# Performance work log

Measured on AMD Instinct MI355X. Metric: run time of the kernel, lower is better.

## Reference

```python
import jax, jax.numpy as jnp
import numpy as np

B, C, F = 16384, 1000, 256
ALPHA = 10


def setup_inputs() -> dict:
    key = jax.random.key(0)
    k1, k2, k3, k4, k5 = jax.random.split(key, 5)
    logits = jax.random.normal(k1, (B, C), dtype=jnp.float32)
    features = jax.random.normal(k2, (B, F), dtype=jnp.float32)
    mean_vecs = jax.random.normal(k3, (C, F), dtype=jnp.float32)
    # Per-class Weibull (shape, loc, scale) as fit by scipy.weibull_min.fit.
    wb_shape = jax.random.uniform(k4, (C,), dtype=jnp.float32, minval=1.0, maxval=4.0)
    wb_loc = jnp.zeros((C,), dtype=jnp.float32)
    # typical tail distance for randn features/means is ~sqrt(2F) ~ 22.6
    wb_scale = jax.random.uniform(k5, (C,), dtype=jnp.float32, minval=10.0, maxval=25.0)
    return {"logits": logits, "features": features, "mean_vecs": mean_vecs,
            "wb_shape": wb_shape, "wb_loc": wb_loc, "wb_scale": wb_scale}


def reference(logits, features, mean_vecs, wb_shape, wb_loc, wb_scale):
    # Batched per-class Euclidean distances via the GEMM identity
    # ||f - m||^2 = ||f||^2 + ||m||^2 - 2 f.m  (avoids [B,C,F] intermediate).
    f2 = jnp.sum(features * features, axis=1, keepdims=True)        # [B,1]
    m2 = jnp.sum(mean_vecs * mean_vecs, axis=1)                     # [C]
    d2 = f2 + m2[None, :] - 2.0 * (features @ mean_vecs.T)          # [B,C]
    dist = jnp.sqrt(jnp.maximum(d2, 1e-12))                         # [B,C]
    # Analytic weibull_min CDF: 1 - exp(-((x - loc)/scale)^c), 0 for x <= loc.
    xp = (dist - wb_loc[None, :]) / wb_scale[None, :]
    pos = xp > 0
    xp_safe = jnp.where(pos, xp, 1.0)
    w = jnp.where(pos, 1.0 - jnp.exp(-(xp_safe ** wb_shape[None, :])), 0.0)
    # OpenMax reweighting + softmax (exp/sum-normalize as in the original).
    scores = logits * (1.0 - w ** ALPHA)                            # [B,C]
    return jax.nn.softmax(scores, axis=-1)
```

## Files before the change

kernel.cpp:

```cpp
#include <hip/hip_runtime.h>

#define NB 16384
#define NC 1000
#define NF 256
#define SE_STRIDE 1004

typedef _Float16 half8 __attribute__((ext_vector_type(8)));
typedef _Float16 half4v __attribute__((ext_vector_type(4)));
typedef float f32x4 __attribute__((ext_vector_type(4)));

__global__ __launch_bounds__(256) void prep_kernel(
    const float* __restrict__ mean_vecs,
    const float* __restrict__ wb_shape,
    const float* __restrict__ wb_loc,
    const float* __restrict__ wb_scale,
    _Float16* __restrict__ m16f,
    float* __restrict__ pm2,
    float* __restrict__ psh,
    float* __restrict__ pli,
    float* __restrict__ pis)
{
    const int lane = threadIdx.x & 63;
    const int W = blockIdx.x * 4 + (threadIdx.x >> 6);

    if (W < 512) {
        const int gt = W >> 3, kk = W & 7;
        int cls = gt * 16 + (lane & 15);
        if (cls > NC - 1) cls = NC - 1;
        const float* src = mean_vecs + (size_t)cls * NF + kk * 32 + (lane >> 4) * 8;
        const float4 lo = *(const float4*)src;
        const float4 hi = *(const float4*)(src + 4);
        half8 h;
        h[0]=(_Float16)lo.x; h[1]=(_Float16)lo.y; h[2]=(_Float16)lo.z; h[3]=(_Float16)lo.w;
        h[4]=(_Float16)hi.x; h[5]=(_Float16)hi.y; h[6]=(_Float16)hi.z; h[7]=(_Float16)hi.w;
        *((half8*)m16f + (size_t)W * 64 + lane) = h;
    }
    if (W < NC) {
        const float4 v = *((const float4*)(mean_vecs + (size_t)W * NF) + lane);
        float s = v.x*v.x + v.y*v.y + v.z*v.z + v.w*v.w;
        #pragma unroll
        for (int off = 1; off < 64; off <<= 1) s += __shfl_xor(s, off, 64);
        if (lane == 0) {
            const float isc = 1.0f / wb_scale[W];
            pm2[W] = s;
            psh[W] = wb_shape[W];
            pli[W] = wb_loc[W] * isc;
            pis[W] = isc;
        }
    }
}

__global__ __launch_bounds__(512, 4) void score_kernel(
    const float* __restrict__ logits,
    const float* __restrict__ features,
    const _Float16* __restrict__ m16f,
    const float* __restrict__ pm2,
    const float* __restrict__ psh,
    const float* __restrict__ pli,
    const float* __restrict__ pis,
    float* __restrict__ out)
{
    __shared__ _Float16 sfeat[8][512];
    __shared__ _Float16 se[16][SE_STRIDE];
    __shared__ float sp[4][1024];
    __shared__ float sf2[16];

    const int lane = threadIdx.x & 63;
    const int wave = threadIdx.x >> 6;
    const int q    = lane >> 4;
    const int mr   = lane & 15;
    const int row  = blockIdx.x * 16 + mr;

    const half8* mbase = (const half8*)m16f + (size_t)(wave * 8) * 8 * 64 + lane;

    half8 aA[8], aB[8];
    #pragma unroll
    for (int kk = 0; kk < 8; ++kk) aA[kk] = mbase[kk * 64];
    #pragma unroll
    for (int kk = 0; kk < 8; ++kk) aB[kk] = mbase[(8 + kk) * 64];

    {
        const int t = threadIdx.x;
        if (t < 256) {
            ((float4*)&sp[0][0])[t] = ((const float4*)pm2)[t];
            ((float4*)&sp[2][0])[t] = ((const float4*)pli)[t];
        } else {
            const int u = t - 256;
            ((float4*)&sp[1][0])[u] = ((const float4*)psh)[u];
            ((float4*)&sp[3][0])[u] = ((const float4*)pis)[u];
        }
    }

    {
        const float* src = features + (size_t)(blockIdx.x * 16 + mr) * NF
                         + wave * 32 + q * 8;
        const float4 lo = *(const float4*)src;
        const float4 hi = *(const float4*)(src + 4);
        half8 h;
        h[0]=(_Float16)lo.x; h[1]=(_Float16)lo.y; h[2]=(_Float16)lo.z; h[3]=(_Float16)lo.w;
        h[4]=(_Float16)hi.x; h[5]=(_Float16)hi.y; h[6]=(_Float16)hi.z; h[7]=(_Float16)hi.w;
        *(half8*)&sfeat[wave][lane * 8] = h;
    }

    if (wave == 0) {
        float f2l = 0.f;
        const float* fb = features + (size_t)row * NF;
        #pragma unroll
        for (int kk = 0; kk < 8; ++kk) {
            const float4* p = (const float4*)(fb + kk * 32 + q * 8);
            const float4 lo = p[0], hi = p[1];
            f2l += lo.x*lo.x + lo.y*lo.y + lo.z*lo.z + lo.w*lo.w
                 + hi.x*hi.x + hi.y*hi.y + hi.z*hi.z + hi.w*hi.w;
        }
        f2l += __shfl_xor(f2l, 16, 64);
        f2l += __shfl_xor(f2l, 32, 64);
        if (lane < 16) sf2[lane] = f2l;
    }

    __syncthreads();

    const float f2 = sf2[mr];
    const float NL2E = -1.44269504088896340736f;
    const float LOG2E = 1.44269504088896340736f;

#define TILE_BODY(T, BUF)                                                     \
    do {                                                                      \
        const int cb   = (wave * 8 + (T)) * 16 + q * 4;                       \
        const bool cvg = (cb <= NC - 4);                                      \
        const int cbc  = cvg ? cb : (NC - 4);                                 \
        f32x4 acc0 = {0.f, 0.f, 0.f, 0.f};                                    \
        f32x4 acc1 = {0.f, 0.f, 0.f, 0.f};                                    \
        _Pragma("unroll")                                                     \
        for (int kk = 0; kk < 4; ++kk) {                                      \
            const half8 b0 = *(const half8*)&sfeat[kk][lane * 8];             \
            const half8 b1 = *(const half8*)&sfeat[kk + 4][lane * 8];         \
            acc0 = __builtin_amdgcn_mfma_f32_16x16x32_f16(BUF[kk],     b0, acc0, 0, 0, 0); \
            acc1 = __builtin_amdgcn_mfma_f32_16x16x32_f16(BUF[kk + 4], b1, acc1, 0, 0, 0); \
        }                                                                     \
        if ((T) + 2 < 8) {                                                    \
            _Pragma("unroll")                                                 \
            for (int kk = 0; kk < 8; ++kk)                                    \
                BUF[kk] = mbase[(size_t)(((T) + 2) * 8 + kk) * 64];           \
        }                                                                     \
        const f32x4 m2v = *(const f32x4*)&sp[0][cbc];                         \
        const f32x4 shv = *(const f32x4*)&sp[1][cbc];                         \
        const f32x4 liv = *(const f32x4*)&sp[2][cbc];                         \
        const f32x4 iv  = *(const f32x4*)&sp[3][cbc];                         \
        half4v oh;                                                            \
        _Pragma("unroll")                                                     \
        for (int j = 0; j < 4; ++j) {                                         \
            float av   = acc0[j] + acc1[j];                                   \
            float d2   = fmaxf(f2 + m2v[j] - 2.0f * av, 1e-12f);              \
            float dist = __builtin_amdgcn_sqrtf(d2);                          \
            float xp   = dist * iv[j] - liv[j];                               \
            float xs   = fmaxf(xp, 1e-30f);                                   \
            float tt   = __builtin_amdgcn_exp2f(                              \
                             shv[j] * __builtin_amdgcn_logf(xs));             \
            float w    = 1.0f - __builtin_amdgcn_exp2f(NL2E * tt);            \
            w = (xp > 0.f) ? w : 0.f;                                         \
            float w2 = w * w, w4 = w2 * w2, w8 = w4 * w4;                     \
            oh[j] = (_Float16)(1.0f - w8 * w2);                               \
        }                                                                     \
        if (cvg)                                                              \
            *(half4v*)&se[mr][cb] = oh;                                       \
    } while (0)

    TILE_BODY(0, aA);
    TILE_BODY(1, aB);
    TILE_BODY(2, aA);
    TILE_BODY(3, aB);
    TILE_BODY(4, aA);
    TILE_BODY(5, aB);
    TILE_BODY(6, aA);
    TILE_BODY(7, aB);
#undef TILE_BODY

    float4 lgp[2][4];
    #pragma unroll
    for (int rr = 0; rr < 2; ++rr) {
        const size_t grow = (size_t)(blockIdx.x * 16 + wave * 2 + rr);
        const float* lrow = logits + grow * NC;
        #pragma unroll
        for (int i = 0; i < 4; ++i) {
            const int idx = i * 64 + lane;
            if (idx < 250) {
                float4 l4 = *(const float4*)(lrow + idx * 4);
                l4.x *= LOG2E; l4.y *= LOG2E; l4.z *= LOG2E; l4.w *= LOG2E;
                lgp[rr][i] = l4;
            }
        }
    }

    __syncthreads();

    #pragma unroll
    for (int rr = 0; rr < 2; ++rr) {
        const int r = wave * 2 + rr;
        const size_t grow = (size_t)(blockIdx.x * 16 + r);

        float4 ev[4];
        float psum = 0.f;
        #pragma unroll
        for (int i = 0; i < 4; ++i) {
            const int idx = i * 64 + lane;
            if (idx < 250) {
                const half4v g4 = *(const half4v*)&se[r][idx * 4];
                const float4 l4 = lgp[rr][i];
                float4 e4;
                e4.x = __builtin_amdgcn_exp2f(l4.x * (float)g4[0]);
                e4.y = __builtin_amdgcn_exp2f(l4.y * (float)g4[1]);
                e4.z = __builtin_amdgcn_exp2f(l4.z * (float)g4[2]);
                e4.w = __builtin_amdgcn_exp2f(l4.w * (float)g4[3]);
                ev[i] = e4;
                psum += (e4.x + e4.y) + (e4.z + e4.w);
            }
        }
        #pragma unroll
        for (int off = 1; off < 64; off <<= 1)
            psum += __shfl_xor(psum, off, 64);
        const float inv = 1.0f / psum;

        float* orow = out + grow * NC;
        #pragma unroll
        for (int i = 0; i < 4; ++i) {
            const int idx = i * 64 + lane;
            if (idx < 250) {
                float4 v = ev[i];
                v.x *= inv; v.y *= inv; v.z *= inv; v.w *= inv;
                *(float4*)(orow + idx * 4) = v;
            }
        }
    }
}

extern "C" void kernel_launch(void* const* d_in, const int* in_sizes, int n_in,
                              void* d_out, int out_size, void* d_ws, size_t ws_size,
                              hipStream_t stream) {
    const float* logits    = (const float*)d_in[0];
    const float* features  = (const float*)d_in[1];
    const float* mean_vecs = (const float*)d_in[2];
    const float* wb_shape  = (const float*)d_in[3];
    const float* wb_loc    = (const float*)d_in[4];
    const float* wb_scale  = (const float*)d_in[5];
    float* out = (float*)d_out;

    _Float16* m16f = (_Float16*)d_ws;
    float* pm2 = (float*)((char*)d_ws + 524288);
    float* psh = (float*)((char*)d_ws + 524288 + 4096);
    float* pli = (float*)((char*)d_ws + 524288 + 8192);
    float* pis = (float*)((char*)d_ws + 524288 + 12288);

    prep_kernel<<<252, 256, 0, stream>>>(mean_vecs, wb_shape, wb_loc, wb_scale,
                                         m16f, pm2, psh, pli, pis);
    score_kernel<<<NB / 16, 512, 0, stream>>>(logits, features, m16f,
                                              pm2, psh, pli, pis, out);
}
```

Before: 156.3 us.

## Parallelize feature norm over four waves, raise MFMA priority, use nontemporal output stores

The per-row squared-norm computation moves from a single wave to four waves, each reducing four rows with coalesced float4 loads and xor shuffles. This shortens the serial prologue before the barrier. The MFMA section is wrapped in s_setprio raise and lower calls so matrix work gets issue priority over other waves. The output softmax rows are written with nontemporal stores to avoid polluting cache with write-once data. These are three independent micro-optimizations, and each has a small, uncertain effect.

```diff
diff --git a/kernel.cpp b/kernel.cpp
--- a/kernel.cpp
+++ b/kernel.cpp
@@ -69,7 +69,6 @@
     const int wave = threadIdx.x >> 6;
     const int q    = lane >> 4;
     const int mr   = lane & 15;
-    const int row  = blockIdx.x * 16 + mr;
 
     const half8* mbase = (const half8*)m16f + (size_t)(wave * 8) * 8 * 64 + lane;
 
@@ -102,19 +101,22 @@
         *(half8*)&sfeat[wave][lane * 8] = h;
     }
 
-    if (wave == 0) {
-        float f2l = 0.f;
-        const float* fb = features + (size_t)row * NF;
-        #pragma unroll
-        for (int kk = 0; kk < 8; ++kk) {
-            const float4* p = (const float4*)(fb + kk * 32 + q * 8);
-            const float4 lo = p[0], hi = p[1];
-            f2l += lo.x*lo.x + lo.y*lo.y + lo.z*lo.z + lo.w*lo.w
-                 + hi.x*hi.x + hi.y*hi.y + hi.z*hi.z + hi.w*hi.w;
-        }
-        f2l += __shfl_xor(f2l, 16, 64);
-        f2l += __shfl_xor(f2l, 32, 64);
-        if (lane < 16) sf2[lane] = f2l;
+    if (wave < 4) {
+        const int r   = wave * 4 + (lane >> 4);
+        const int c16 = lane & 15;
+        const float4* fb = (const float4*)(features
+                          + (size_t)(blockIdx.x * 16 + r) * NF) + c16 * 4;
+        float s = 0.f;
+        #pragma unroll
+        for (int i = 0; i < 4; ++i) {
+            const float4 v = fb[i];
+            s += v.x*v.x + v.y*v.y + v.z*v.z + v.w*v.w;
+        }
+        s += __shfl_xor(s, 1, 64);
+        s += __shfl_xor(s, 2, 64);
+        s += __shfl_xor(s, 4, 64);
+        s += __shfl_xor(s, 8, 64);
+        if (c16 == 0) sf2[r] = s;
     }
 
     __syncthreads();
@@ -130,6 +132,7 @@
         const int cbc  = cvg ? cb : (NC - 4);                                 \
         f32x4 acc0 = {0.f, 0.f, 0.f, 0.f};                                    \
         f32x4 acc1 = {0.f, 0.f, 0.f, 0.f};                                    \
+        __builtin_amdgcn_s_setprio(1);                                        \
         _Pragma("unroll")                                                     \
         for (int kk = 0; kk < 4; ++kk) {                                      \
             const half8 b0 = *(const half8*)&sfeat[kk][lane * 8];             \
@@ -137,6 +140,7 @@
             acc0 = __builtin_amdgcn_mfma_f32_16x16x32_f16(BUF[kk],     b0, acc0, 0, 0, 0); \
             acc1 = __builtin_amdgcn_mfma_f32_16x16x32_f16(BUF[kk + 4], b1, acc1, 0, 0, 0); \
         }                                                                     \
+        __builtin_amdgcn_s_setprio(0);                                        \
         if ((T) + 2 < 8) {                                                    \
             _Pragma("unroll")                                                 \
             for (int kk = 0; kk < 8; ++kk)                                    \
@@ -225,9 +229,10 @@
         for (int i = 0; i < 4; ++i) {
             const int idx = i * 64 + lane;
             if (idx < 250) {
-                float4 v = ev[i];
-                v.x *= inv; v.y *= inv; v.z *= inv; v.w *= inv;
-                *(float4*)(orow + idx * 4) = v;
+                f32x4 sv;
+                sv[0] = ev[i].x * inv; sv[1] = ev[i].y * inv;
+                sv[2] = ev[i].z * inv; sv[3] = ev[i].w * inv;
+                __builtin_nontemporal_store(sv, (f32x4*)(orow + idx * 4));
             }
         }
     }
```

Result: faster. 151.7 us (-2.9%).
